# Kernel tuning notes

Measured on AMD Instinct MI355X. Metric: run time of the kernel, lower is better.

The kernel has to match this reference:

```python
import jax, jax.numpy as jnp
import numpy as np

B, N, H = 4, 1024, 64

def setup_inputs() -> dict:
    key = jax.random.key(0)
    k1, k2, k3 = jax.random.split(key, 3)
    x = jax.random.normal(k1, (B, N, H), dtype=jnp.float32)
    # nn.Linear(2H, H): weight [H, 2H], bias [H]
    s1 = 1.0 / np.sqrt(2 * H)
    W1 = jax.random.uniform(k2, (H, 2 * H), minval=-s1, maxval=s1, dtype=jnp.float32)
    b1 = jnp.zeros((H,), dtype=jnp.float32)
    # nn.Linear(H, 1): weight [1, H], bias [1]
    s2 = 1.0 / np.sqrt(H)
    W2 = jax.random.uniform(k3, (1, H), minval=-s2, maxval=s2, dtype=jnp.float32)
    b2 = jnp.zeros((1,), dtype=jnp.float32)
    return {"x": x, "W1": W1, "b1": b1, "W2": W2, "b2": b2}

def reference(x, W1, b1, W2, b2):
    # cat([x_i, x_j]) @ W1.T == x_i @ W1a.T + x_j @ W1b.T  (decomposed; same math)
    W1a, W1b = W1[:, :x.shape[-1]], W1[:, x.shape[-1]:]
    hi = jnp.einsum('bid,hd->bih', x, W1a)            # [B,N,H]
    hj = jnp.einsum('bjd,hd->bjh', x, W1b)            # [B,N,H]
    h = jax.nn.relu(hi[:, :, None, :] + hj[:, None, :, :] + b1)  # [B,N,N,H]
    logits = jnp.einsum('bijh,h->bij', h, W2[0]) + b2[0]          # [B,N,N]
    attn = jax.nn.softmax(logits, axis=-1)
    updated = jnp.einsum('bij,bjd->bid', attn, x)     # [B,N,H]
    return updated, attn
```

## Files before the change

kernel.cpp:

```cpp
#include <hip/hip_runtime.h>

#define ATTN_OFF 262144

#define WS_HIP  0
#define WS_HJP  131072
#define WS_L16  262144
#define WS_SMAX 2359296
#define WS_SSUM 2424832
#define WS_PART 2490368

typedef float4 f4;
typedef _Float16 h2v __attribute__((ext_vector_type(2)));

union F4H { f4 f; h2v h[4]; };
union F2H { float2 f; h2v h[2]; };

__device__ __forceinline__ f4 ld4(const float* p) { return *reinterpret_cast<const f4*>(p); }
__device__ __forceinline__ void st4(float* p, f4 v) { *reinterpret_cast<f4*>(p) = v; }
__device__ __forceinline__ float fdot2f(h2v a, h2v b, float c) {
    return __builtin_amdgcn_fdot2(a, b, c, false);
}
__device__ __forceinline__ h2v pack2(float a, float b) {
    h2v r; r.x = (_Float16)a; r.y = (_Float16)b; return r;
}

__global__ __launch_bounds__(256, 4)
void ka_proj(const float* __restrict__ x, const float* __restrict__ W1,
             const float* __restrict__ b1,
             h2v* __restrict__ hiP, h2v* __restrict__ hjP) {
    __shared__ float xT[64 * 68];
    __shared__ float w1T[64 * 68];
    const int t  = threadIdx.x;
    const int i0 = blockIdx.x * 64;
    const int b  = blockIdx.y;
    const int z  = blockIdx.z;
    const int lo = t & 15;
    const int dq = t >> 4;
#pragma unroll
    for (int p = 0; p < 4; ++p) {
        const int il = p * 16 + lo;
        f4 v = ld4(&x[(size_t)(b * 1024 + i0 + il) * 64 + dq * 4]);
        xT[(dq * 4 + 0) * 68 + il] = v.x;
        xT[(dq * 4 + 1) * 68 + il] = v.y;
        xT[(dq * 4 + 2) * 68 + il] = v.z;
        xT[(dq * 4 + 3) * 68 + il] = v.w;
        f4 w = ld4(&W1[(size_t)il * 128 + z * 64 + dq * 4]);
        w1T[(dq * 4 + 0) * 68 + il] = w.x;
        w1T[(dq * 4 + 1) * 68 + il] = w.y;
        w1T[(dq * 4 + 2) * 68 + il] = w.z;
        w1T[(dq * 4 + 3) * 68 + il] = w.w;
    }
    __syncthreads();
    const int tx = t & 15;
    const int ty = t >> 4;
    float acc[4][4];
    if (z == 0) {
        f4 bv = ld4(&b1[tx * 4]);
        float ba[4] = {bv.x, bv.y, bv.z, bv.w};
#pragma unroll
        for (int ii = 0; ii < 4; ++ii)
#pragma unroll
            for (int cc = 0; cc < 4; ++cc) acc[ii][cc] = ba[cc];
    } else {
#pragma unroll
        for (int ii = 0; ii < 4; ++ii)
#pragma unroll
            for (int cc = 0; cc < 4; ++cc) acc[ii][cc] = 0.f;
    }
#pragma unroll 8
    for (int d = 0; d < 64; ++d) {
        f4 xv = ld4(&xT[d * 68 + ty * 4]);
        f4 wv = ld4(&w1T[d * 68 + tx * 4]);
        float xa[4] = {xv.x, xv.y, xv.z, xv.w};
        float wa[4] = {wv.x, wv.y, wv.z, wv.w};
#pragma unroll
        for (int ii = 0; ii < 4; ++ii)
#pragma unroll
            for (int cc = 0; cc < 4; ++cc)
                acc[ii][cc] = fmaf(xa[ii], wa[cc], acc[ii][cc]);
    }
    h2v* outp = z ? hjP : hiP;
#pragma unroll
    for (int p = 0; p < 2; ++p) {
        F4H u;
#pragma unroll
        for (int ii = 0; ii < 4; ++ii)
            u.h[ii] = pack2(acc[ii][p * 2 + 0], acc[ii][p * 2 + 1]);
        st4((float*)&outp[(size_t)(b * 32 + tx * 2 + p) * 1024 + i0 + ty * 4], u.f);
    }
}

__global__ __launch_bounds__(256, 4)
void kb_logits(const h2v* __restrict__ hiP, const h2v* __restrict__ hjP,
               const float* __restrict__ W2, _Float16* __restrict__ l16,
               float* __restrict__ smax, float* __restrict__ ssum) {
    __shared__ __align__(16) h2v s_hi[32 * 128];
    __shared__ __align__(16) h2v s_hj[32 * 64];
    __shared__ h2v s_w2[32];
    const int t  = threadIdx.x;
    const int jT = blockIdx.x;
    const int iT = blockIdx.y;
    const int b  = blockIdx.z;
#pragma unroll
    for (int p = 0; p < 4; ++p) {
        const int idx = p * 256 + t;
        const int hp  = idx >> 5;
        const int c4  = (idx & 31) * 4;
        st4((float*)&s_hi[hp * 128 + c4],
            ld4((const float*)&hiP[(size_t)(b * 32 + hp) * 1024 + iT * 128 + c4]));
    }
#pragma unroll
    for (int p = 0; p < 2; ++p) {
        const int idx = p * 256 + t;
        const int hp  = idx >> 4;
        const int c4  = (idx & 15) * 4;
        st4((float*)&s_hj[hp * 64 + c4],
            ld4((const float*)&hjP[(size_t)(b * 32 + hp) * 1024 + jT * 64 + c4]));
    }
    if (t < 16) {
        f4 w = ld4(&W2[t * 4]);
        s_w2[t * 2]     = pack2(w.x, w.y);
        s_w2[t * 2 + 1] = pack2(w.z, w.w);
    }
    __syncthreads();
    const int tx = t & 15;
    const int ty = t >> 4;
    float acc[8][4];
#pragma unroll
    for (int ii = 0; ii < 8; ++ii)
#pragma unroll
        for (int jj = 0; jj < 4; ++jj) acc[ii][jj] = 0.f;
    const h2v z2 = (h2v)0;
#pragma unroll 4
    for (int hp = 0; hp < 32; ++hp) {
        F4H a0, a1, bb;
        a0.f = ld4((const float*)&s_hi[hp * 128 + ty * 8]);
        a1.f = ld4((const float*)&s_hi[hp * 128 + ty * 8 + 4]);
        bb.f = ld4((const float*)&s_hj[hp * 64 + tx * 4]);
        const h2v w2p = s_w2[hp];
#pragma unroll
        for (int ii = 0; ii < 8; ++ii) {
            const h2v av = (ii < 4) ? a0.h[ii] : a1.h[ii - 4];
#pragma unroll
            for (int jj = 0; jj < 4; ++jj) {
                h2v r = __builtin_elementwise_max(av + bb.h[jj], z2);
                acc[ii][jj] = fdot2f(r, w2p, acc[ii][jj]);
            }
        }
    }
#pragma unroll
    for (int ii = 0; ii < 8; ++ii) {
        const int row = b * 1024 + iT * 128 + ty * 8 + ii;
        F2H uo;
        uo.h[0] = pack2(acc[ii][0], acc[ii][1]);
        uo.h[1] = pack2(acc[ii][2], acc[ii][3]);
        *reinterpret_cast<float2*>(&l16[(size_t)row * 1024 + jT * 64 + tx * 4]) = uo.f;
        float m = fmaxf(fmaxf(acc[ii][0], acc[ii][1]), fmaxf(acc[ii][2], acc[ii][3]));
#pragma unroll
        for (int d = 1; d < 16; d <<= 1) m = fmaxf(m, __shfl_xor(m, d));
        float s = __expf(acc[ii][0] - m) + __expf(acc[ii][1] - m) +
                  __expf(acc[ii][2] - m) + __expf(acc[ii][3] - m);
#pragma unroll
        for (int d = 1; d < 16; d <<= 1) s += __shfl_xor(s, d);
        if (tx == 0) {
            smax[jT * 4096 + row] = m;
            ssum[jT * 4096 + row] = s;
        }
    }
}

#define PS 132
__global__ __launch_bounds__(256, 2)
void kd_av(const _Float16* __restrict__ l16, const float* __restrict__ smax,
           const float* __restrict__ ssum, const float* __restrict__ x,
           float* __restrict__ attn, float* __restrict__ part) {
    __shared__ __align__(16) h2v s_p[32 * PS];
    __shared__ __align__(16) h2v s_x[32 * 64];
    __shared__ float s_m[128];
    __shared__ float s_il[128];
    const int t  = threadIdx.x;
    const int ks = blockIdx.x;
    const int iT = blockIdx.y;
    const int b  = blockIdx.z;
    const int j0 = ks * 64;
    const int gr = b * 1024 + iT * 128;
    if (t < 128) {
        float mv[16], sv[16];
#pragma unroll
        for (int c = 0; c < 16; ++c) {
            mv[c] = smax[c * 4096 + gr + t];
            sv[c] = ssum[c * 4096 + gr + t];
        }
        float M = mv[0];
#pragma unroll
        for (int c = 1; c < 16; ++c) M = fmaxf(M, mv[c]);
        float L = 0.f;
#pragma unroll
        for (int c = 0; c < 16; ++c) L += sv[c] * __expf(mv[c] - M);
        s_m[t]  = M;
        s_il[t] = 1.0f / L;
    }
#pragma unroll
    for (int it = 0; it < 2; ++it) {
        const int idx = it * 256 + t;
        const int jp  = idx >> 4;
        const int d4  = (idx & 15) * 4;
        f4 r0 = ld4(&x[(size_t)(b * 1024 + j0 + jp * 2)     * 64 + d4]);
        f4 r1 = ld4(&x[(size_t)(b * 1024 + j0 + jp * 2 + 1) * 64 + d4]);
        F4H u;
        u.h[0] = pack2(r0.x, r1.x); u.h[1] = pack2(r0.y, r1.y);
        u.h[2] = pack2(r0.z, r1.z); u.h[3] = pack2(r0.w, r1.w);
        st4((float*)&s_x[jp * 64 + d4], u.f);
    }
    __syncthreads();
#pragma unroll 2
    for (int it = 0; it < 4; ++it) {
        const int idx = it * 256 + t;
        const int rl  = idx >> 3;
        const int j8  = (idx & 7) * 8;
        F4H u;
        u.f = ld4((const float*)&l16[(size_t)(gr + rl) * 1024 + j0 + j8]);
        const float m  = s_m[rl];
        const float il = s_il[rl];
        float p[8];
#pragma unroll
        for (int k = 0; k < 4; ++k) {
            p[2 * k]     = __expf((float)u.h[k].x - m) * il;
            p[2 * k + 1] = __expf((float)u.h[k].y - m) * il;
        }
        float* ap = &attn[(size_t)(gr + rl) * 1024 + j0 + j8];
        st4(ap,     make_float4(p[0], p[1], p[2], p[3]));
        st4(ap + 4, make_float4(p[4], p[5], p[6], p[7]));
        const int jp0 = (idx & 7) * 4;
#pragma unroll
        for (int k = 0; k < 4; ++k)
            s_p[(jp0 + k) * PS + rl] = pack2(p[2 * k], p[2 * k + 1]);
    }
    __syncthreads();
    const int tx = t & 15;
    const int ty = t >> 4;
    float acc[8][4];
#pragma unroll
    for (int ii = 0; ii < 8; ++ii)
#pragma unroll
        for (int dd = 0; dd < 4; ++dd) acc[ii][dd] = 0.f;
#pragma unroll 4
    for (int jp = 0; jp < 32; ++jp) {
        F4H a0, a1, xv;
        a0.f = ld4((const float*)&s_p[jp * PS + ty * 8]);
        a1.f = ld4((const float*)&s_p[jp * PS + ty * 8 + 4]);
        xv.f = ld4((const float*)&s_x[jp * 64 + tx * 4]);
        h2v aa[8] = {a0.h[0], a0.h[1], a0.h[2], a0.h[3],
                     a1.h[0], a1.h[1], a1.h[2], a1.h[3]};
#pragma unroll
        for (int ii = 0; ii < 8; ++ii)
#pragma unroll
            for (int dd = 0; dd < 4; ++dd)
                acc[ii][dd] = fdot2f(aa[ii], xv.h[dd], acc[ii][dd]);
    }
#pragma unroll
    for (int ii = 0; ii < 8; ++ii) {
        f4 o = make_float4(acc[ii][0], acc[ii][1], acc[ii][2], acc[ii][3]);
        st4(&part[(size_t)(ks * 4096 + gr + ty * 8 + ii) * 64 + tx * 4], o);
    }
}

__global__ __launch_bounds__(256)
void ke_reduce(const float* __restrict__ part, float* __restrict__ out) {
    const int g = blockIdx.x * 256 + threadIdx.x;
    f4 a = ld4(&part[(size_t)g * 4]);
#pragma unroll
    for (int ks = 1; ks < 16; ++ks) {
        f4 v = ld4(&part[(size_t)ks * 262144 + g * 4]);
        a.x += v.x; a.y += v.y; a.z += v.z; a.w += v.w;
    }
    st4(&out[(size_t)g * 4], a);
}

extern "C" void kernel_launch(void* const* d_in, const int* in_sizes, int n_in,
                              void* d_out, int out_size, void* d_ws, size_t ws_size,
                              hipStream_t stream) {
    const float* x  = (const float*)d_in[0];
    const float* W1 = (const float*)d_in[1];
    const float* b1 = (const float*)d_in[2];
    const float* W2 = (const float*)d_in[3];
    float* out = (float*)d_out;
    float* ws  = (float*)d_ws;
    h2v*      hiP  = (h2v*)(ws + WS_HIP);
    h2v*      hjP  = (h2v*)(ws + WS_HJP);
    _Float16* l16  = (_Float16*)(ws + WS_L16);
    float*    smax = ws + WS_SMAX;
    float*    ssum = ws + WS_SSUM;
    float*    part = ws + WS_PART;

    ka_proj  <<<dim3(16, 4, 2), 256, 0, stream>>>(x, W1, b1, hiP, hjP);
    kb_logits<<<dim3(16, 8, 4), 256, 0, stream>>>(hiP, hjP, W2, l16, smax, ssum);
    kd_av    <<<dim3(16, 8, 4), 256, 0, stream>>>(l16, smax, ssum, x,
                                                  out + ATTN_OFF, part);
    ke_reduce<<<dim3(256),      256, 0, stream>>>(part, out);
}
```

Before: 103.9 us.

## Fuse four kernels into one cooperative kernel with grid syncs

Replaces the four separate launches (projection, logits, softmax+AV, reduce) with a single cooperative kernel of 512 blocks that separates the phases with grid.sync(). Shared memory is one byte buffer reused across phases. The aim is to remove per-launch overhead and the gaps between kernels. In exchange, every block must wait at each grid barrier, the projection and reduce phases leave blocks idle, and the launch bounds occupancy of 2 per SM may limit latency hiding in the logits phase.

```diff
diff --git a/kernel.cpp b/kernel.cpp
--- a/kernel.cpp
+++ b/kernel.cpp
@@ -1,4 +1,7 @@
 #include <hip/hip_runtime.h>
+#include <hip/hip_cooperative_groups.h>
+
+namespace cg = cooperative_groups;
 
 #define ATTN_OFF 262144
 
@@ -24,257 +27,263 @@
     h2v r; r.x = (_Float16)a; r.y = (_Float16)b; return r;
 }
 
-__global__ __launch_bounds__(256, 4)
-void ka_proj(const float* __restrict__ x, const float* __restrict__ W1,
-             const float* __restrict__ b1,
-             h2v* __restrict__ hiP, h2v* __restrict__ hjP) {
-    __shared__ float xT[64 * 68];
-    __shared__ float w1T[64 * 68];
-    const int t  = threadIdx.x;
-    const int i0 = blockIdx.x * 64;
-    const int b  = blockIdx.y;
-    const int z  = blockIdx.z;
-    const int lo = t & 15;
-    const int dq = t >> 4;
-#pragma unroll
-    for (int p = 0; p < 4; ++p) {
-        const int il = p * 16 + lo;
-        f4 v = ld4(&x[(size_t)(b * 1024 + i0 + il) * 64 + dq * 4]);
-        xT[(dq * 4 + 0) * 68 + il] = v.x;
-        xT[(dq * 4 + 1) * 68 + il] = v.y;
-        xT[(dq * 4 + 2) * 68 + il] = v.z;
-        xT[(dq * 4 + 3) * 68 + il] = v.w;
-        f4 w = ld4(&W1[(size_t)il * 128 + z * 64 + dq * 4]);
-        w1T[(dq * 4 + 0) * 68 + il] = w.x;
-        w1T[(dq * 4 + 1) * 68 + il] = w.y;
-        w1T[(dq * 4 + 2) * 68 + il] = w.z;
-        w1T[(dq * 4 + 3) * 68 + il] = w.w;
+#define PS 132
+
+__global__ __launch_bounds__(256, 2)
+void fused(const float* __restrict__ x, const float* __restrict__ W1,
+           const float* __restrict__ b1, const float* __restrict__ W2,
+           h2v* __restrict__ hiP, h2v* __restrict__ hjP,
+           _Float16* __restrict__ l16, float* __restrict__ smax,
+           float* __restrict__ ssum, float* __restrict__ part,
+           float* __restrict__ attn, float* __restrict__ out) {
+    cg::grid_group grid = cg::this_grid();
+    __shared__ __align__(16) char smem[34816];
+    const int t   = threadIdx.x;
+    const int bid = blockIdx.x;
+
+    if (bid < 128) {
+        float* xT  = (float*)smem;
+        float* w1T = xT + 64 * 68;
+        const int i0 = (bid & 15) * 64;
+        const int b  = (bid >> 4) & 3;
+        const int z  = bid >> 6;
+        const int lo = t & 15;
+        const int dq = t >> 4;
+#pragma unroll
+        for (int p = 0; p < 4; ++p) {
+            const int il = p * 16 + lo;
+            f4 v = ld4(&x[(size_t)(b * 1024 + i0 + il) * 64 + dq * 4]);
+            xT[(dq * 4 + 0) * 68 + il] = v.x;
+            xT[(dq * 4 + 1) * 68 + il] = v.y;
+            xT[(dq * 4 + 2) * 68 + il] = v.z;
+            xT[(dq * 4 + 3) * 68 + il] = v.w;
+            f4 w = ld4(&W1[(size_t)il * 128 + z * 64 + dq * 4]);
+            w1T[(dq * 4 + 0) * 68 + il] = w.x;
+            w1T[(dq * 4 + 1) * 68 + il] = w.y;
+            w1T[(dq * 4 + 2) * 68 + il] = w.z;
+            w1T[(dq * 4 + 3) * 68 + il] = w.w;
+        }
+        __syncthreads();
+        const int tx = t & 15;
+        const int ty = t >> 4;
+        float acc[4][4];
+        if (z == 0) {
+            f4 bv = ld4(&b1[tx * 4]);
+            float ba[4] = {bv.x, bv.y, bv.z, bv.w};
+#pragma unroll
+            for (int ii = 0; ii < 4; ++ii)
+#pragma unroll
+                for (int cc = 0; cc < 4; ++cc) acc[ii][cc] = ba[cc];
+        } else {
+#pragma unroll
+            for (int ii = 0; ii < 4; ++ii)
+#pragma unroll
+                for (int cc = 0; cc < 4; ++cc) acc[ii][cc] = 0.f;
+        }
+#pragma unroll 8
+        for (int d = 0; d < 64; ++d) {
+            f4 xv = ld4(&xT[d * 68 + ty * 4]);
+            f4 wv = ld4(&w1T[d * 68 + tx * 4]);
+            float xa[4] = {xv.x, xv.y, xv.z, xv.w};
+            float wa[4] = {wv.x, wv.y, wv.z, wv.w};
+#pragma unroll
+            for (int ii = 0; ii < 4; ++ii)
+#pragma unroll
+                for (int cc = 0; cc < 4; ++cc)
+                    acc[ii][cc] = fmaf(xa[ii], wa[cc], acc[ii][cc]);
+        }
+        h2v* outp = z ? hjP : hiP;
+#pragma unroll
+        for (int p = 0; p < 2; ++p) {
+            F4H u;
+#pragma unroll
+            for (int ii = 0; ii < 4; ++ii)
+                u.h[ii] = pack2(acc[ii][p * 2 + 0], acc[ii][p * 2 + 1]);
+            st4((float*)&outp[(size_t)(b * 32 + tx * 2 + p) * 1024 + i0 + ty * 4], u.f);
+        }
     }
-    __syncthreads();
-    const int tx = t & 15;
-    const int ty = t >> 4;
-    float acc[4][4];
-    if (z == 0) {
-        f4 bv = ld4(&b1[tx * 4]);
-        float ba[4] = {bv.x, bv.y, bv.z, bv.w};
-#pragma unroll
-        for (int ii = 0; ii < 4; ++ii)
-#pragma unroll
-            for (int cc = 0; cc < 4; ++cc) acc[ii][cc] = ba[cc];
-    } else {
-#pragma unroll
-        for (int ii = 0; ii < 4; ++ii)
-#pragma unroll
-            for (int cc = 0; cc < 4; ++cc) acc[ii][cc] = 0.f;
+    grid.sync();
+
+    {
+        h2v* s_hi = (h2v*)smem;
+        h2v* s_hj = s_hi + 32 * 128;
+        h2v* s_w2 = s_hj + 32 * 64;
+        const int jT = bid & 15;
+        const int iT = (bid >> 4) & 7;
+        const int b  = bid >> 7;
+#pragma unroll
+        for (int p = 0; p < 4; ++p) {
+            const int idx = p * 256 + t;
+            const int hp  = idx >> 5;
+            const int c4  = (idx & 31) * 4;
+            st4((float*)&s_hi[hp * 128 + c4],
+                ld4((const float*)&hiP[(size_t)(b * 32 + hp) * 1024 + iT * 128 + c4]));
+        }
+#pragma unroll
+        for (int p = 0; p < 2; ++p) {
+            const int idx = p * 256 + t;
+            const int hp  = idx >> 4;
+            const int c4  = (idx & 15) * 4;
+            st4((float*)&s_hj[hp * 64 + c4],
+                ld4((const float*)&hjP[(size_t)(b * 32 + hp) * 1024 + jT * 64 + c4]));
+        }
+        if (t < 16) {
+            f4 w = ld4(&W2[t * 4]);
+            s_w2[t * 2]     = pack2(w.x, w.y);
+            s_w2[t * 2 + 1] = pack2(w.z, w.w);
+        }
+        __syncthreads();
+        const int tx = t & 15;
+        const int ty = t >> 4;
+        float acc[8][4];
+#pragma unroll
+        for (int ii = 0; ii < 8; ++ii)
+#pragma unroll
+            for (int jj = 0; jj < 4; ++jj) acc[ii][jj] = 0.f;
+        const h2v z2 = (h2v)0;
+#pragma unroll 4
+        for (int hp = 0; hp < 32; ++hp) {
+            F4H a0, a1, bb;
+            a0.f = ld4((const float*)&s_hi[hp * 128 + ty * 8]);
+            a1.f = ld4((const float*)&s_hi[hp * 128 + ty * 8 + 4]);
+            bb.f = ld4((const float*)&s_hj[hp * 64 + tx * 4]);
+            const h2v w2p = s_w2[hp];
+#pragma unroll
+            for (int ii = 0; ii < 8; ++ii) {
+                const h2v av = (ii < 4) ? a0.h[ii] : a1.h[ii - 4];
+#pragma unroll
+                for (int jj = 0; jj < 4; ++jj) {
+                    h2v r = __builtin_elementwise_max(av + bb.h[jj], z2);
+                    acc[ii][jj] = fdot2f(r, w2p, acc[ii][jj]);
+                }
+            }
+        }
+#pragma unroll
+        for (int ii = 0; ii < 8; ++ii) {
+            const int row = b * 1024 + iT * 128 + ty * 8 + ii;
+            F2H uo;
+            uo.h[0] = pack2(acc[ii][0], acc[ii][1]);
+            uo.h[1] = pack2(acc[ii][2], acc[ii][3]);
+            *reinterpret_cast<float2*>(&l16[(size_t)row * 1024 + jT * 64 + tx * 4]) = uo.f;
+            float m = fmaxf(fmaxf(acc[ii][0], acc[ii][1]), fmaxf(acc[ii][2], acc[ii][3]));
+#pragma unroll
+            for (int d = 1; d < 16; d <<= 1) m = fmaxf(m, __shfl_xor(m, d));
+            float s = __expf(acc[ii][0] - m) + __expf(acc[ii][1] - m) +
+                      __expf(acc[ii][2] - m) + __expf(acc[ii][3] - m);
+#pragma unroll
+            for (int d = 1; d < 16; d <<= 1) s += __shfl_xor(s, d);
+            if (tx == 0) {
+                smax[jT * 4096 + row] = m;
+                ssum[jT * 4096 + row] = s;
+            }
+        }
     }
-#pragma unroll 8
-    for (int d = 0; d < 64; ++d) {
-        f4 xv = ld4(&xT[d * 68 + ty * 4]);
-        f4 wv = ld4(&w1T[d * 68 + tx * 4]);
-        float xa[4] = {xv.x, xv.y, xv.z, xv.w};
-        float wa[4] = {wv.x, wv.y, wv.z, wv.w};
-#pragma unroll
-        for (int ii = 0; ii < 4; ++ii)
-#pragma unroll
-            for (int cc = 0; cc < 4; ++cc)
-                acc[ii][cc] = fmaf(xa[ii], wa[cc], acc[ii][cc]);
+    grid.sync();
+
+    {
+        h2v*   s_p  = (h2v*)smem;
+        h2v*   s_x  = s_p + 32 * PS;
+        float* s_m  = (float*)(s_x + 32 * 64);
+        float* s_il = s_m + 128;
+        const int ks = bid & 15;
+        const int iT = (bid >> 4) & 7;
+        const int b  = bid >> 7;
+        const int j0 = ks * 64;
+        const int gr = b * 1024 + iT * 128;
+        if (t < 128) {
+            float mv[16], sv[16];
+#pragma unroll
+            for (int c = 0; c < 16; ++c) {
+                mv[c] = smax[c * 4096 + gr + t];
+                sv[c] = ssum[c * 4096 + gr + t];
+            }
+            float M = mv[0];
+#pragma unroll
+            for (int c = 1; c < 16; ++c) M = fmaxf(M, mv[c]);
+            float L = 0.f;
+#pragma unroll
+            for (int c = 0; c < 16; ++c) L += sv[c] * __expf(mv[c] - M);
+            s_m[t]  = M;
+            s_il[t] = 1.0f / L;
+        }
+#pragma unroll
+        for (int it = 0; it < 2; ++it) {
+            const int idx = it * 256 + t;
+            const int jp  = idx >> 4;
+            const int d4  = (idx & 15) * 4;
+            f4 r0 = ld4(&x[(size_t)(b * 1024 + j0 + jp * 2)     * 64 + d4]);
+            f4 r1 = ld4(&x[(size_t)(b * 1024 + j0 + jp * 2 + 1) * 64 + d4]);
+            F4H u;
+            u.h[0] = pack2(r0.x, r1.x); u.h[1] = pack2(r0.y, r1.y);
+            u.h[2] = pack2(r0.z, r1.z); u.h[3] = pack2(r0.w, r1.w);
+            st4((float*)&s_x[jp * 64 + d4], u.f);
+        }
+        __syncthreads();
+#pragma unroll 2
+        for (int it = 0; it < 4; ++it) {
+            const int idx = it * 256 + t;
+            const int rl  = idx >> 3;
+            const int j8  = (idx & 7) * 8;
+            F4H u;
+            u.f = ld4((const float*)&l16[(size_t)(gr + rl) * 1024 + j0 + j8]);
+            const float m  = s_m[rl];
+            const float il = s_il[rl];
+            float p[8];
+#pragma unroll
+            for (int k = 0; k < 4; ++k) {
+                p[2 * k]     = __expf((float)u.h[k].x - m) * il;
+                p[2 * k + 1] = __expf((float)u.h[k].y - m) * il;
+            }
+            float* ap = &attn[(size_t)(gr + rl) * 1024 + j0 + j8];
+            st4(ap,     make_float4(p[0], p[1], p[2], p[3]));
+            st4(ap + 4, make_float4(p[4], p[5], p[6], p[7]));
+            const int jp0 = (idx & 7) * 4;
+#pragma unroll
+            for (int k = 0; k < 4; ++k)
+                s_p[(jp0 + k) * PS + rl] = pack2(p[2 * k], p[2 * k + 1]);
+        }
+        __syncthreads();
+        const int tx = t & 15;
+        const int ty = t >> 4;
+        float acc[8][4];
+#pragma unroll
+        for (int ii = 0; ii < 8; ++ii)
+#pragma unroll
+            for (int dd = 0; dd < 4; ++dd) acc[ii][dd] = 0.f;
+#pragma unroll 4
+        for (int jp = 0; jp < 32; ++jp) {
+            F4H a0, a1, xv;
+            a0.f = ld4((const float*)&s_p[jp * PS + ty * 8]);
+            a1.f = ld4((const float*)&s_p[jp * PS + ty * 8 + 4]);
+            xv.f = ld4((const float*)&s_x[jp * 64 + tx * 4]);
+            h2v aa[8] = {a0.h[0], a0.h[1], a0.h[2], a0.h[3],
+                         a1.h[0], a1.h[1], a1.h[2], a1.h[3]};
+#pragma unroll
+            for (int ii = 0; ii < 8; ++ii)
+#pragma unroll
+                for (int dd = 0; dd < 4; ++dd)
+                    acc[ii][dd] = fdot2f(aa[ii], xv.h[dd], acc[ii][dd]);
+        }
+#pragma unroll
+        for (int ii = 0; ii < 8; ++ii) {
+            f4 o = make_float4(acc[ii][0], acc[ii][1], acc[ii][2], acc[ii][3]);
+            st4(&part[(size_t)(ks * 4096 + gr + ty * 8 + ii) * 64 + tx * 4], o);
+        }
     }
-    h2v* outp = z ? hjP : hiP;
-#pragma unroll
-    for (int p = 0; p < 2; ++p) {
-        F4H u;
-#pragma unroll
-        for (int ii = 0; ii < 4; ++ii)
-            u.h[ii] = pack2(acc[ii][p * 2 + 0], acc[ii][p * 2 + 1]);
-        st4((float*)&outp[(size_t)(b * 32 + tx * 2 + p) * 1024 + i0 + ty * 4], u.f);
+    grid.sync();
+
+    {
+        const int idx = bid * 256 + t;
+        if (idx < 65536) {
+            f4 a = ld4(&part[(size_t)idx * 4]);
+#pragma unroll
+            for (int ks = 1; ks < 16; ++ks) {
+                f4 v = ld4(&part[(size_t)ks * 262144 + idx * 4]);
+                a.x += v.x; a.y += v.y; a.z += v.z; a.w += v.w;
+            }
+            st4(&out[(size_t)idx * 4], a);
+        }
     }
-}
-
-__global__ __launch_bounds__(256, 4)
-void kb_logits(const h2v* __restrict__ hiP, const h2v* __restrict__ hjP,
-               const float* __restrict__ W2, _Float16* __restrict__ l16,
-               float* __restrict__ smax, float* __restrict__ ssum) {
-    __shared__ __align__(16) h2v s_hi[32 * 128];
-    __shared__ __align__(16) h2v s_hj[32 * 64];
-    __shared__ h2v s_w2[32];
-    const int t  = threadIdx.x;
-    const int jT = blockIdx.x;
-    const int iT = blockIdx.y;
-    const int b  = blockIdx.z;
-#pragma unroll
-    for (int p = 0; p < 4; ++p) {
-        const int idx = p * 256 + t;
-        const int hp  = idx >> 5;
-        const int c4  = (idx & 31) * 4;
-        st4((float*)&s_hi[hp * 128 + c4],
-            ld4((const float*)&hiP[(size_t)(b * 32 + hp) * 1024 + iT * 128 + c4]));
-    }
-#pragma unroll
-    for (int p = 0; p < 2; ++p) {
-        const int idx = p * 256 + t;
-        const int hp  = idx >> 4;
-        const int c4  = (idx & 15) * 4;
-        st4((float*)&s_hj[hp * 64 + c4],
-            ld4((const float*)&hjP[(size_t)(b * 32 + hp) * 1024 + jT * 64 + c4]));
-    }
-    if (t < 16) {
-        f4 w = ld4(&W2[t * 4]);
-        s_w2[t * 2]     = pack2(w.x, w.y);
-        s_w2[t * 2 + 1] = pack2(w.z, w.w);
-    }
-    __syncthreads();
-    const int tx = t & 15;
-    const int ty = t >> 4;
-    float acc[8][4];
-#pragma unroll
-    for (int ii = 0; ii < 8; ++ii)
-#pragma unroll
-        for (int jj = 0; jj < 4; ++jj) acc[ii][jj] = 0.f;
-    const h2v z2 = (h2v)0;
-#pragma unroll 4
-    for (int hp = 0; hp < 32; ++hp) {
-        F4H a0, a1, bb;
-        a0.f = ld4((const float*)&s_hi[hp * 128 + ty * 8]);
-        a1.f = ld4((const float*)&s_hi[hp * 128 + ty * 8 + 4]);
-        bb.f = ld4((const float*)&s_hj[hp * 64 + tx * 4]);
-        const h2v w2p = s_w2[hp];
-#pragma unroll
-        for (int ii = 0; ii < 8; ++ii) {
-            const h2v av = (ii < 4) ? a0.h[ii] : a1.h[ii - 4];
-#pragma unroll
-            for (int jj = 0; jj < 4; ++jj) {
-                h2v r = __builtin_elementwise_max(av + bb.h[jj], z2);
-                acc[ii][jj] = fdot2f(r, w2p, acc[ii][jj]);
-            }
-        }
-    }
-#pragma unroll
-    for (int ii = 0; ii < 8; ++ii) {
-        const int row = b * 1024 + iT * 128 + ty * 8 + ii;
-        F2H uo;
-        uo.h[0] = pack2(acc[ii][0], acc[ii][1]);
-        uo.h[1] = pack2(acc[ii][2], acc[ii][3]);
-        *reinterpret_cast<float2*>(&l16[(size_t)row * 1024 + jT * 64 + tx * 4]) = uo.f;
-        float m = fmaxf(fmaxf(acc[ii][0], acc[ii][1]), fmaxf(acc[ii][2], acc[ii][3]));
-#pragma unroll
-        for (int d = 1; d < 16; d <<= 1) m = fmaxf(m, __shfl_xor(m, d));
-        float s = __expf(acc[ii][0] - m) + __expf(acc[ii][1] - m) +
-                  __expf(acc[ii][2] - m) + __expf(acc[ii][3] - m);
-#pragma unroll
-        for (int d = 1; d < 16; d <<= 1) s += __shfl_xor(s, d);
-        if (tx == 0) {
-            smax[jT * 4096 + row] = m;
-            ssum[jT * 4096 + row] = s;
-        }
-    }
-}
-
-#define PS 132
-__global__ __launch_bounds__(256, 2)
-void kd_av(const _Float16* __restrict__ l16, const float* __restrict__ smax,
-           const float* __restrict__ ssum, const float* __restrict__ x,
-           float* __restrict__ attn, float* __restrict__ part) {
-    __shared__ __align__(16) h2v s_p[32 * PS];
-    __shared__ __align__(16) h2v s_x[32 * 64];
-    __shared__ float s_m[128];
-    __shared__ float s_il[128];
-    const int t  = threadIdx.x;
-    const int ks = blockIdx.x;
-    const int iT = blockIdx.y;
-    const int b  = blockIdx.z;
-    const int j0 = ks * 64;
-    const int gr = b * 1024 + iT * 128;
-    if (t < 128) {
-        float mv[16], sv[16];
-#pragma unroll
-        for (int c = 0; c < 16; ++c) {
-            mv[c] = smax[c * 4096 + gr + t];
-            sv[c] = ssum[c * 4096 + gr + t];
-        }
-        float M = mv[0];
-#pragma unroll
-        for (int c = 1; c < 16; ++c) M = fmaxf(M, mv[c]);
-        float L = 0.f;
-#pragma unroll
-        for (int c = 0; c < 16; ++c) L += sv[c] * __expf(mv[c] - M);
-        s_m[t]  = M;
-        s_il[t] = 1.0f / L;
-    }
-#pragma unroll
-    for (int it = 0; it < 2; ++it) {
-        const int idx = it * 256 + t;
-        const int jp  = idx >> 4;
-        const int d4  = (idx & 15) * 4;
-        f4 r0 = ld4(&x[(size_t)(b * 1024 + j0 + jp * 2)     * 64 + d4]);
-        f4 r1 = ld4(&x[(size_t)(b * 1024 + j0 + jp * 2 + 1) * 64 + d4]);
-        F4H u;
-        u.h[0] = pack2(r0.x, r1.x); u.h[1] = pack2(r0.y, r1.y);
-        u.h[2] = pack2(r0.z, r1.z); u.h[3] = pack2(r0.w, r1.w);
-        st4((float*)&s_x[jp * 64 + d4], u.f);
-    }
-    __syncthreads();
-#pragma unroll 2
-    for (int it = 0; it < 4; ++it) {
-        const int idx = it * 256 + t;
-        const int rl  = idx >> 3;
-        const int j8  = (idx & 7) * 8;
-        F4H u;
-        u.f = ld4((const float*)&l16[(size_t)(gr + rl) * 1024 + j0 + j8]);
-        const float m  = s_m[rl];
-        const float il = s_il[rl];
-        float p[8];
-#pragma unroll
-        for (int k = 0; k < 4; ++k) {
-            p[2 * k]     = __expf((float)u.h[k].x - m) * il;
-            p[2 * k + 1] = __expf((float)u.h[k].y - m) * il;
-        }
-        float* ap = &attn[(size_t)(gr + rl) * 1024 + j0 + j8];
-        st4(ap,     make_float4(p[0], p[1], p[2], p[3]));
-        st4(ap + 4, make_float4(p[4], p[5], p[6], p[7]));
-        const int jp0 = (idx & 7) * 4;
-#pragma unroll
-        for (int k = 0; k < 4; ++k)
-            s_p[(jp0 + k) * PS + rl] = pack2(p[2 * k], p[2 * k + 1]);
-    }
-    __syncthreads();
-    const int tx = t & 15;
-    const int ty = t >> 4;
-    float acc[8][4];
-#pragma unroll
-    for (int ii = 0; ii < 8; ++ii)
-#pragma unroll
-        for (int dd = 0; dd < 4; ++dd) acc[ii][dd] = 0.f;
-#pragma unroll 4
-    for (int jp = 0; jp < 32; ++jp) {
-        F4H a0, a1, xv;
-        a0.f = ld4((const float*)&s_p[jp * PS + ty * 8]);
-        a1.f = ld4((const float*)&s_p[jp * PS + ty * 8 + 4]);
-        xv.f = ld4((const float*)&s_x[jp * 64 + tx * 4]);
-        h2v aa[8] = {a0.h[0], a0.h[1], a0.h[2], a0.h[3],
-                     a1.h[0], a1.h[1], a1.h[2], a1.h[3]};
-#pragma unroll
-        for (int ii = 0; ii < 8; ++ii)
-#pragma unroll
-            for (int dd = 0; dd < 4; ++dd)
-                acc[ii][dd] = fdot2f(aa[ii], xv.h[dd], acc[ii][dd]);
-    }
-#pragma unroll
-    for (int ii = 0; ii < 8; ++ii) {
-        f4 o = make_float4(acc[ii][0], acc[ii][1], acc[ii][2], acc[ii][3]);
-        st4(&part[(size_t)(ks * 4096 + gr + ty * 8 + ii) * 64 + tx * 4], o);
-    }
-}
-
-__global__ __launch_bounds__(256)
-void ke_reduce(const float* __restrict__ part, float* __restrict__ out) {
-    const int g = blockIdx.x * 256 + threadIdx.x;
-    f4 a = ld4(&part[(size_t)g * 4]);
-#pragma unroll
-    for (int ks = 1; ks < 16; ++ks) {
-        f4 v = ld4(&part[(size_t)ks * 262144 + g * 4]);
-        a.x += v.x; a.y += v.y; a.z += v.z; a.w += v.w;
-    }
-    st4(&out[(size_t)g * 4], a);
 }
 
 extern "C" void kernel_launch(void* const* d_in, const int* in_sizes, int n_in,
@@ -292,10 +301,11 @@
     float*    smax = ws + WS_SMAX;
     float*    ssum = ws + WS_SSUM;
     float*    part = ws + WS_PART;
-
-    ka_proj  <<<dim3(16, 4, 2), 256, 0, stream>>>(x, W1, b1, hiP, hjP);
-    kb_logits<<<dim3(16, 8, 4), 256, 0, stream>>>(hiP, hjP, W2, l16, smax, ssum);
-    kd_av    <<<dim3(16, 8, 4), 256, 0, stream>>>(l16, smax, ssum, x,
-                                                  out + ATTN_OFF, part);
-    ke_reduce<<<dim3(256),      256, 0, stream>>>(part, out);
+    float*    attn = out + ATTN_OFF;
+
+    void* args[] = {(void*)&x, (void*)&W1, (void*)&b1, (void*)&W2,
+                    (void*)&hiP, (void*)&hjP, (void*)&l16, (void*)&smax,
+                    (void*)&ssum, (void*)&part, (void*)&attn, (void*)&out};
+    hipLaunchCooperativeKernel((const void*)fused, dim3(512), dim3(256),
+                               args, 0, stream);
 }
```

Measured after the change: 288.6 us. 178% more time.

## Fuse split-K reduction into AV kernel via atomic last-block counters

Applied to the files above, without the earlier changes.

Removes the separate reduction kernel launch by having each kd_av block bump per-16-row-group atomic counters after writing its partial sums. The block that arrives last for a group sums the 16 partials and writes the output. Counters are zeroed in the projection kernel. This saves a launch and its tail, at the cost of fences, atomics and a serialized reduction tail inside the last-arriving blocks.

```diff
diff --git a/kernel.cpp b/kernel.cpp
--- a/kernel.cpp
+++ b/kernel.cpp
@@ -7,7 +7,8 @@
 #define WS_L16  262144
 #define WS_SMAX 2359296
 #define WS_SSUM 2424832
-#define WS_PART 2490368
+#define WS_CNT  2490368
+#define WS_PART 2490624
 
 typedef float4 f4;
 typedef _Float16 h2v __attribute__((ext_vector_type(2)));
@@ -27,13 +28,15 @@
 __global__ __launch_bounds__(256, 4)
 void ka_proj(const float* __restrict__ x, const float* __restrict__ W1,
              const float* __restrict__ b1,
-             h2v* __restrict__ hiP, h2v* __restrict__ hjP) {
+             h2v* __restrict__ hiP, h2v* __restrict__ hjP,
+             unsigned int* __restrict__ cnt) {
     __shared__ float xT[64 * 68];
     __shared__ float w1T[64 * 68];
     const int t  = threadIdx.x;
     const int i0 = blockIdx.x * 64;
     const int b  = blockIdx.y;
     const int z  = blockIdx.z;
+    if (blockIdx.x == 0 && b == 0 && z == 0) cnt[t] = 0u;
     const int lo = t & 15;
     const int dq = t >> 4;
 #pragma unroll
@@ -173,17 +176,20 @@
 __global__ __launch_bounds__(256, 2)
 void kd_av(const _Float16* __restrict__ l16, const float* __restrict__ smax,
            const float* __restrict__ ssum, const float* __restrict__ x,
-           float* __restrict__ attn, float* __restrict__ part) {
+           float* __restrict__ attn, float* __restrict__ part,
+           unsigned int* __restrict__ cnt, float* __restrict__ out) {
     __shared__ __align__(16) h2v s_p[32 * PS];
     __shared__ __align__(16) h2v s_x[32 * 64];
     __shared__ float s_m[128];
     __shared__ float s_il[128];
+    __shared__ unsigned int s_won;
     const int t  = threadIdx.x;
     const int ks = blockIdx.x;
     const int iT = blockIdx.y;
     const int b  = blockIdx.z;
     const int j0 = ks * 64;
     const int gr = b * 1024 + iT * 128;
+    if (t == 0) s_won = 0u;
     if (t < 128) {
         float mv[16], sv[16];
 #pragma unroll
@@ -263,18 +269,31 @@
         f4 o = make_float4(acc[ii][0], acc[ii][1], acc[ii][2], acc[ii][3]);
         st4(&part[(size_t)(ks * 4096 + gr + ty * 8 + ii) * 64 + tx * 4], o);
     }
-}
-
-__global__ __launch_bounds__(256)
-void ke_reduce(const float* __restrict__ part, float* __restrict__ out) {
-    const int g = blockIdx.x * 256 + threadIdx.x;
-    f4 a = ld4(&part[(size_t)g * 4]);
-#pragma unroll
-    for (int ks = 1; ks < 16; ++ks) {
-        f4 v = ld4(&part[(size_t)ks * 262144 + g * 4]);
-        a.x += v.x; a.y += v.y; a.z += v.z; a.w += v.w;
-    }
-    st4(&out[(size_t)g * 4], a);
+    __threadfence();
+    __syncthreads();
+    if (t < 8) {
+        const int creg = (b * 8 + iT) * 8 + t;
+        const unsigned int old = atomicAdd(&cnt[creg], 1u);
+        if (old == 15u) atomicOr(&s_won, 1u << t);
+    }
+    __syncthreads();
+    const unsigned int won = s_won;
+    if (won == 0u) return;
+    __threadfence();
+#pragma unroll 1
+    for (int s = 0; s < 8; ++s) {
+        if (!(won & (1u << s))) continue;
+        const int row = gr + s * 16 + (t >> 4);
+        const int d4  = (t & 15) * 4;
+        const size_t o = (size_t)row * 64 + d4;
+        f4 a = ld4(&part[o]);
+#pragma unroll
+        for (int k = 1; k < 16; ++k) {
+            f4 v = ld4(&part[(size_t)k * 262144 + o]);
+            a.x += v.x; a.y += v.y; a.z += v.z; a.w += v.w;
+        }
+        st4(&out[o], a);
+    }
 }
 
 extern "C" void kernel_launch(void* const* d_in, const int* in_sizes, int n_in,
@@ -286,16 +305,16 @@
     const float* W2 = (const float*)d_in[3];
     float* out = (float*)d_out;
     float* ws  = (float*)d_ws;
-    h2v*      hiP  = (h2v*)(ws + WS_HIP);
-    h2v*      hjP  = (h2v*)(ws + WS_HJP);
-    _Float16* l16  = (_Float16*)(ws + WS_L16);
-    float*    smax = ws + WS_SMAX;
-    float*    ssum = ws + WS_SSUM;
-    float*    part = ws + WS_PART;
-
-    ka_proj  <<<dim3(16, 4, 2), 256, 0, stream>>>(x, W1, b1, hiP, hjP);
+    h2v*          hiP  = (h2v*)(ws + WS_HIP);
+    h2v*          hjP  = (h2v*)(ws + WS_HJP);
+    _Float16*     l16  = (_Float16*)(ws + WS_L16);
+    float*        smax = ws + WS_SMAX;
+    float*        ssum = ws + WS_SSUM;
+    unsigned int* cnt  = (unsigned int*)(ws + WS_CNT);
+    float*        part = ws + WS_PART;
+
+    ka_proj  <<<dim3(16, 4, 2), 256, 0, stream>>>(x, W1, b1, hiP, hjP, cnt);
     kb_logits<<<dim3(16, 8, 4), 256, 0, stream>>>(hiP, hjP, W2, l16, smax, ssum);
     kd_av    <<<dim3(16, 8, 4), 256, 0, stream>>>(l16, smax, ssum, x,
-                                                  out + ATTN_OFF, part);
-    ke_reduce<<<dim3(256),      256, 0, stream>>>(part, out);
-}
+                                                  out + ATTN_OFF, part, cnt, out);
+}
```

Result: slower. 183.5 us (+76.6%).

## Store locally-normalized exp tiles and rescale per chunk; halve partial-sum precision

Applied to the files above, without the earlier changes.

The logits kernel now stores exp(logit - local tile max) in fp16 instead of raw fp16 logits. The AV kernel then applies a single per-row, per-chunk scale factor instead of recomputing exp for every element. It also folds that scale into the partial AV results and writes them as fp16, which halves the traffic into the reduction kernel. This removes transcendental work and memory bandwidth from the second pass, at the cost of extra fp16 rounding in the probabilities and partials.

```diff
diff --git a/kernel.cpp b/kernel.cpp
--- a/kernel.cpp
+++ b/kernel.cpp
@@ -4,7 +4,7 @@
 
 #define WS_HIP  0
 #define WS_HJP  131072
-#define WS_L16  262144
+#define WS_P16  262144
 #define WS_SMAX 2359296
 #define WS_SSUM 2424832
 #define WS_PART 2490368
@@ -92,7 +92,7 @@
 
 __global__ __launch_bounds__(256, 4)
 void kb_logits(const h2v* __restrict__ hiP, const h2v* __restrict__ hjP,
-               const float* __restrict__ W2, _Float16* __restrict__ l16,
+               const float* __restrict__ W2, _Float16* __restrict__ p16,
                float* __restrict__ smax, float* __restrict__ ssum) {
     __shared__ __align__(16) h2v s_hi[32 * 128];
     __shared__ __align__(16) h2v s_hj[32 * 64];
@@ -151,15 +151,16 @@
 #pragma unroll
     for (int ii = 0; ii < 8; ++ii) {
         const int row = b * 1024 + iT * 128 + ty * 8 + ii;
+        float m = fmaxf(fmaxf(acc[ii][0], acc[ii][1]), fmaxf(acc[ii][2], acc[ii][3]));
+#pragma unroll
+        for (int d = 1; d < 16; d <<= 1) m = fmaxf(m, __shfl_xor(m, d));
+        float p0 = __expf(acc[ii][0] - m), p1 = __expf(acc[ii][1] - m);
+        float p2 = __expf(acc[ii][2] - m), p3 = __expf(acc[ii][3] - m);
         F2H uo;
-        uo.h[0] = pack2(acc[ii][0], acc[ii][1]);
-        uo.h[1] = pack2(acc[ii][2], acc[ii][3]);
-        *reinterpret_cast<float2*>(&l16[(size_t)row * 1024 + jT * 64 + tx * 4]) = uo.f;
-        float m = fmaxf(fmaxf(acc[ii][0], acc[ii][1]), fmaxf(acc[ii][2], acc[ii][3]));
-#pragma unroll
-        for (int d = 1; d < 16; d <<= 1) m = fmaxf(m, __shfl_xor(m, d));
-        float s = __expf(acc[ii][0] - m) + __expf(acc[ii][1] - m) +
-                  __expf(acc[ii][2] - m) + __expf(acc[ii][3] - m);
+        uo.h[0] = pack2(p0, p1);
+        uo.h[1] = pack2(p2, p3);
+        *reinterpret_cast<float2*>(&p16[(size_t)row * 1024 + jT * 64 + tx * 4]) = uo.f;
+        float s = p0 + p1 + p2 + p3;
 #pragma unroll
         for (int d = 1; d < 16; d <<= 1) s += __shfl_xor(s, d);
         if (tx == 0) {
@@ -171,13 +172,12 @@
 
 #define PS 132
 __global__ __launch_bounds__(256, 2)
-void kd_av(const _Float16* __restrict__ l16, const float* __restrict__ smax,
+void kd_av(const _Float16* __restrict__ p16, const float* __restrict__ smax,
            const float* __restrict__ ssum, const float* __restrict__ x,
-           float* __restrict__ attn, float* __restrict__ part) {
+           float* __restrict__ attn, h2v* __restrict__ part16) {
     __shared__ __align__(16) h2v s_p[32 * PS];
     __shared__ __align__(16) h2v s_x[32 * 64];
-    __shared__ float s_m[128];
-    __shared__ float s_il[128];
+    __shared__ float s_sc[128];
     const int t  = threadIdx.x;
     const int ks = blockIdx.x;
     const int iT = blockIdx.y;
@@ -197,8 +197,7 @@
         float L = 0.f;
 #pragma unroll
         for (int c = 0; c < 16; ++c) L += sv[c] * __expf(mv[c] - M);
-        s_m[t]  = M;
-        s_il[t] = 1.0f / L;
+        s_sc[t] = __expf(mv[ks] - M) / L;
     }
 #pragma unroll
     for (int it = 0; it < 2; ++it) {
@@ -219,22 +218,17 @@
         const int rl  = idx >> 3;
         const int j8  = (idx & 7) * 8;
         F4H u;
-        u.f = ld4((const float*)&l16[(size_t)(gr + rl) * 1024 + j0 + j8]);
-        const float m  = s_m[rl];
-        const float il = s_il[rl];
-        float p[8];
-#pragma unroll
-        for (int k = 0; k < 4; ++k) {
-            p[2 * k]     = __expf((float)u.h[k].x - m) * il;
-            p[2 * k + 1] = __expf((float)u.h[k].y - m) * il;
-        }
+        u.f = ld4((const float*)&p16[(size_t)(gr + rl) * 1024 + j0 + j8]);
+        const float sc = s_sc[rl];
         float* ap = &attn[(size_t)(gr + rl) * 1024 + j0 + j8];
-        st4(ap,     make_float4(p[0], p[1], p[2], p[3]));
-        st4(ap + 4, make_float4(p[4], p[5], p[6], p[7]));
+        st4(ap, make_float4((float)u.h[0].x * sc, (float)u.h[0].y * sc,
+                            (float)u.h[1].x * sc, (float)u.h[1].y * sc));
+        st4(ap + 4, make_float4((float)u.h[2].x * sc, (float)u.h[2].y * sc,
+                                (float)u.h[3].x * sc, (float)u.h[3].y * sc));
         const int jp0 = (idx & 7) * 4;
 #pragma unroll
         for (int k = 0; k < 4; ++k)
-            s_p[(jp0 + k) * PS + rl] = pack2(p[2 * k], p[2 * k + 1]);
+            s_p[(jp0 + k) * PS + rl] = u.h[k];
     }
     __syncthreads();
     const int tx = t & 15;
@@ -260,19 +254,28 @@
     }
 #pragma unroll
     for (int ii = 0; ii < 8; ++ii) {
-        f4 o = make_float4(acc[ii][0], acc[ii][1], acc[ii][2], acc[ii][3]);
-        st4(&part[(size_t)(ks * 4096 + gr + ty * 8 + ii) * 64 + tx * 4], o);
+        const float sc = s_sc[ty * 8 + ii];
+        F2H o;
+        o.h[0] = pack2(acc[ii][0] * sc, acc[ii][1] * sc);
+        o.h[1] = pack2(acc[ii][2] * sc, acc[ii][3] * sc);
+        *reinterpret_cast<float2*>(
+            &part16[(size_t)(ks * 4096 + gr + ty * 8 + ii) * 32 + tx * 2]) = o.f;
     }
 }
 
 __global__ __launch_bounds__(256)
-void ke_reduce(const float* __restrict__ part, float* __restrict__ out) {
-    const int g = blockIdx.x * 256 + threadIdx.x;
-    f4 a = ld4(&part[(size_t)g * 4]);
-#pragma unroll
-    for (int ks = 1; ks < 16; ++ks) {
-        f4 v = ld4(&part[(size_t)ks * 262144 + g * 4]);
-        a.x += v.x; a.y += v.y; a.z += v.z; a.w += v.w;
+void ke_reduce(const h2v* __restrict__ part16, float* __restrict__ out) {
+    const int g   = blockIdx.x * 256 + threadIdx.x;
+    const int row = g >> 4;
+    const int dp  = (g & 15) * 2;
+    f4 a = make_float4(0.f, 0.f, 0.f, 0.f);
+#pragma unroll
+    for (int ks = 0; ks < 16; ++ks) {
+        F2H v;
+        v.f = *reinterpret_cast<const float2*>(
+            &part16[(size_t)(ks * 4096 + row) * 32 + dp]);
+        a.x += (float)v.h[0].x; a.y += (float)v.h[0].y;
+        a.z += (float)v.h[1].x; a.w += (float)v.h[1].y;
     }
     st4(&out[(size_t)g * 4], a);
 }
@@ -288,14 +291,14 @@
     float* ws  = (float*)d_ws;
     h2v*      hiP  = (h2v*)(ws + WS_HIP);
     h2v*      hjP  = (h2v*)(ws + WS_HJP);
-    _Float16* l16  = (_Float16*)(ws + WS_L16);
+    _Float16* p16  = (_Float16*)(ws + WS_P16);
     float*    smax = ws + WS_SMAX;
     float*    ssum = ws + WS_SSUM;
-    float*    part = ws + WS_PART;
+    h2v*      part = (h2v*)(ws + WS_PART);
 
     ka_proj  <<<dim3(16, 4, 2), 256, 0, stream>>>(x, W1, b1, hiP, hjP);
-    kb_logits<<<dim3(16, 8, 4), 256, 0, stream>>>(hiP, hjP, W2, l16, smax, ssum);
-    kd_av    <<<dim3(16, 8, 4), 256, 0, stream>>>(l16, smax, ssum, x,
+    kb_logits<<<dim3(16, 8, 4), 256, 0, stream>>>(hiP, hjP, W2, p16, smax, ssum);
+    kd_av    <<<dim3(16, 8, 4), 256, 0, stream>>>(p16, smax, ssum, x,
                                                   out + ATTN_OFF, part);
     ke_reduce<<<dim3(256),      256, 0, stream>>>(part, out);
 }
```

Measured after the change: 107.0 us. +3.0%, slower.
